# Kernel tuning notes

Measured on AMD Instinct MI355X. Metric: run time of the kernel, lower is better.

## Reference

```python
import jax, jax.numpy as jnp
import numpy as np

B, S, D = 32, 2048, 512
NUM_SEG = 65  # mask//100 in [0, 64]; segment 0 is padding, dropped from output


def setup_inputs() -> dict:
    key = jax.random.key(0)
    k1, k2 = jax.random.split(key)
    output = jax.random.normal(k1, (B, S, D), dtype=jnp.float32)
    mask = jax.random.randint(k2, (B, S), 0, 6500, dtype=jnp.int64)
    return {"output": output, "mask": mask}


def reference(output, mask):
    # torch_scatter.scatter_mean(src=output, index=mask//100, dim=-2)[:, 1:, :]
    seg = mask // 100  # [B, S] segment ids in [0, NUM_SEG)
    sums = jax.vmap(
        lambda o, s: jax.ops.segment_sum(o, s, num_segments=NUM_SEG)
    )(output, seg)  # [B, NUM_SEG, D]
    counts = jax.vmap(
        lambda s: jax.ops.segment_sum(
            jnp.ones(s.shape, dtype=output.dtype), s, num_segments=NUM_SEG
        )
    )(seg)  # [B, NUM_SEG]
    # scatter_mean yields 0 for empty segments; clamping count to 1 preserves that
    mean = sums / jnp.maximum(counts, 1.0)[..., None]
    return mean[:, 1:, :]  # drop segment 0 (padding), -> [B, NUM_SEG-1, D]
```

## Files before the change

kernel.cpp:

```cpp
#include <hip/hip_runtime.h>


constexpr int S = 2048;
constexpr int D = 512;
constexpr int NSEG_OUT = 64;

__global__ __launch_bounds__(256, 8) void seg_mean_kernel(
    const float* __restrict__ src,
    const int* __restrict__ mask,
    float* __restrict__ dst) {
  const int segm1 = blockIdx.x;
  const int b = blockIdx.y;
  const int tid = threadIdx.x;
  const unsigned char myseg = (unsigned char)(segm1 + 1);

  __shared__ unsigned char seg_lds[S];
  __shared__ short list[S];
  __shared__ int mcount;
  __shared__ float combine[D];

  const int4* m4 = (const int4*)(mask + (size_t)b * S);
  #pragma unroll
  for (int it = 0; it < (S / 4) / 256; ++it) {
    const int i = it * 256 + tid;
    const int4 v = m4[i];
    seg_lds[i * 4 + 0] = (unsigned char)(v.x / 100);
    seg_lds[i * 4 + 1] = (unsigned char)(v.y / 100);
    seg_lds[i * 4 + 2] = (unsigned char)(v.z / 100);
    seg_lds[i * 4 + 3] = (unsigned char)(v.w / 100);
  }
  __syncthreads();

  if (tid < 64) {
    int cnt = 0;
    for (int base = 0; base < S; base += 64) {
      const bool match = (seg_lds[base + tid] == myseg);
      const unsigned long long bal = __ballot(match);
      if (match) {
        const int pos = __popcll(bal & ((1ull << tid) - 1ull));
        list[cnt + pos] = (short)(base + tid);
      }
      cnt += __popcll(bal);
    }
    if (tid == 0) mcount = cnt;
  }
  __syncthreads();

  const int m = mcount;
  const int h = tid >> 7;
  const int dt = tid & 127;

  const float4* row4 = (const float4*)(src + (size_t)b * S * D);
  float4 acc = make_float4(0.f, 0.f, 0.f, 0.f);

  int i = h;
  for (; i + 2 < m; i += 4) {
    const int s0 = list[i];
    const int s1 = list[i + 2];
    const float4 v0 = row4[(size_t)s0 * (D / 4) + dt];
    const float4 v1 = row4[(size_t)s1 * (D / 4) + dt];
    acc.x += v0.x; acc.y += v0.y; acc.z += v0.z; acc.w += v0.w;
    acc.x += v1.x; acc.y += v1.y; acc.z += v1.z; acc.w += v1.w;
  }
  if (i < m) {
    const int s0 = list[i];
    const float4 v0 = row4[(size_t)s0 * (D / 4) + dt];
    acc.x += v0.x; acc.y += v0.y; acc.z += v0.z; acc.w += v0.w;
  }

  if (h == 1) {
    ((float4*)combine)[dt] = acc;
  }
  __syncthreads();
  if (h == 0) {
    const float4 o = ((float4*)combine)[dt];
    const float inv = 1.0f / fmaxf((float)m, 1.0f);
    float4 r;
    r.x = (acc.x + o.x) * inv;
    r.y = (acc.y + o.y) * inv;
    r.z = (acc.z + o.z) * inv;
    r.w = (acc.w + o.w) * inv;
    float4* out4 = (float4*)(dst + ((size_t)b * NSEG_OUT + segm1) * D);
    out4[dt] = r;
  }
}

extern "C" void kernel_launch(void* const* d_in, const int* in_sizes, int n_in,
                              void* d_out, int out_size, void* d_ws, size_t ws_size,
                              hipStream_t stream) {
  const float* src = (const float*)d_in[0];
  const int* mask = (const int*)d_in[1];
  float* dst = (float*)d_out;

  dim3 grid(NSEG_OUT, 32);
  seg_mean_kernel<<<grid, 256, 0, stream>>>(src, mask, dst);
}
```

Baseline: 28.98 us.

## Split segment scan and row gather per wavefront to drop block barriers

Each of the four wavefronts now scans its own quarter of the mask with register ballots and builds a private row list, then sums those rows across the full D width. The shared-memory segment-id staging and two block-wide barriers before the gather are removed, leaving one barrier before a final four-way reduction in LDS. The cost is a serial per-match loop in each wave to build the list, plus unbalanced work when matches cluster in one quarter.

```diff
diff --git a/kernel.cpp b/kernel.cpp
--- a/kernel.cpp
+++ b/kernel.cpp
@@ -3,6 +3,7 @@
 
 constexpr int S = 2048;
 constexpr int D = 512;
+constexpr int D4 = D / 4;
 constexpr int NSEG_OUT = 64;
 
 __global__ __launch_bounds__(256, 8) void seg_mean_kernel(
@@ -12,76 +13,88 @@
   const int segm1 = blockIdx.x;
   const int b = blockIdx.y;
   const int tid = threadIdx.x;
-  const unsigned char myseg = (unsigned char)(segm1 + 1);
+  const int w = tid >> 6;
+  const int lane = tid & 63;
+  const int myseg = segm1 + 1;
 
-  __shared__ unsigned char seg_lds[S];
-  __shared__ short list[S];
-  __shared__ int mcount;
-  __shared__ float combine[D];
+  __shared__ float sums[4][D];
+  __shared__ short list[4][512];
+  __shared__ int wcnt[4];
 
-  const int4* m4 = (const int4*)(mask + (size_t)b * S);
+  const int4* m4 = (const int4*)(mask + (size_t)b * S) + (size_t)w * 128;
+  const int4 q0 = m4[lane];
+  const int4 q1 = m4[64 + lane];
+
+  unsigned long long bal[8];
+  bal[0] = __ballot(q0.x / 100 == myseg);
+  bal[1] = __ballot(q0.y / 100 == myseg);
+  bal[2] = __ballot(q0.z / 100 == myseg);
+  bal[3] = __ballot(q0.w / 100 == myseg);
+  bal[4] = __ballot(q1.x / 100 == myseg);
+  bal[5] = __ballot(q1.y / 100 == myseg);
+  bal[6] = __ballot(q1.z / 100 == myseg);
+  bal[7] = __ballot(q1.w / 100 == myseg);
+
+  int cnt = 0;
   #pragma unroll
-  for (int it = 0; it < (S / 4) / 256; ++it) {
-    const int i = it * 256 + tid;
-    const int4 v = m4[i];
-    seg_lds[i * 4 + 0] = (unsigned char)(v.x / 100);
-    seg_lds[i * 4 + 1] = (unsigned char)(v.y / 100);
-    seg_lds[i * 4 + 2] = (unsigned char)(v.z / 100);
-    seg_lds[i * 4 + 3] = (unsigned char)(v.w / 100);
+  for (int r = 0; r < 8; ++r) {
+    unsigned long long bb = bal[r];
+    const int sb = 512 * w + 256 * (r >> 2) + (r & 3);
+    while (bb) {
+      const int L = __ffsll((long long)bb) - 1;
+      bb &= bb - 1;
+      if (lane == 0) list[w][cnt] = (short)(sb + 4 * L);
+      ++cnt;
+    }
   }
+  if (lane == 0) wcnt[w] = cnt;
+
+  const float4* row4 = (const float4*)(src + (size_t)b * S * D);
+  float4 a0 = make_float4(0.f, 0.f, 0.f, 0.f);
+  float4 a1 = make_float4(0.f, 0.f, 0.f, 0.f);
+
+  int i = 0;
+  for (; i + 1 < cnt; i += 2) {
+    const int s0 = list[w][i];
+    const int s1 = list[w][i + 1];
+    const float4* r0 = row4 + (size_t)s0 * D4;
+    const float4* r1 = row4 + (size_t)s1 * D4;
+    const float4 v00 = r0[lane];
+    const float4 v01 = r0[64 + lane];
+    const float4 v10 = r1[lane];
+    const float4 v11 = r1[64 + lane];
+    a0.x += v00.x; a0.y += v00.y; a0.z += v00.z; a0.w += v00.w;
+    a1.x += v01.x; a1.y += v01.y; a1.z += v01.z; a1.w += v01.w;
+    a0.x += v10.x; a0.y += v10.y; a0.z += v10.z; a0.w += v10.w;
+    a1.x += v11.x; a1.y += v11.y; a1.z += v11.z; a1.w += v11.w;
+  }
+  if (i < cnt) {
+    const int s0 = list[w][i];
+    const float4* r0 = row4 + (size_t)s0 * D4;
+    const float4 v00 = r0[lane];
+    const float4 v01 = r0[64 + lane];
+    a0.x += v00.x; a0.y += v00.y; a0.z += v00.z; a0.w += v00.w;
+    a1.x += v01.x; a1.y += v01.y; a1.z += v01.z; a1.w += v01.w;
+  }
+
+  ((float4*)sums[w])[lane] = a0;
+  ((float4*)sums[w])[64 + lane] = a1;
   __syncthreads();
 
-  if (tid < 64) {
-    int cnt = 0;
-    for (int base = 0; base < S; base += 64) {
-      const bool match = (seg_lds[base + tid] == myseg);
-      const unsigned long long bal = __ballot(match);
-      if (match) {
-        const int pos = __popcll(bal & ((1ull << tid) - 1ull));
-        list[cnt + pos] = (short)(base + tid);
-      }
-      cnt += __popcll(bal);
-    }
-    if (tid == 0) mcount = cnt;
-  }
-  __syncthreads();
-
-  const int m = mcount;
-  const int h = tid >> 7;
-  const int dt = tid & 127;
-
-  const float4* row4 = (const float4*)(src + (size_t)b * S * D);
-  float4 acc = make_float4(0.f, 0.f, 0.f, 0.f);
-
-  int i = h;
-  for (; i + 2 < m; i += 4) {
-    const int s0 = list[i];
-    const int s1 = list[i + 2];
-    const float4 v0 = row4[(size_t)s0 * (D / 4) + dt];
-    const float4 v1 = row4[(size_t)s1 * (D / 4) + dt];
-    acc.x += v0.x; acc.y += v0.y; acc.z += v0.z; acc.w += v0.w;
-    acc.x += v1.x; acc.y += v1.y; acc.z += v1.z; acc.w += v1.w;
-  }
-  if (i < m) {
-    const int s0 = list[i];
-    const float4 v0 = row4[(size_t)s0 * (D / 4) + dt];
-    acc.x += v0.x; acc.y += v0.y; acc.z += v0.z; acc.w += v0.w;
-  }
-
-  if (h == 1) {
-    ((float4*)combine)[dt] = acc;
-  }
-  __syncthreads();
-  if (h == 0) {
-    const float4 o = ((float4*)combine)[dt];
+  if (tid < D4) {
+    const int m = wcnt[0] + wcnt[1] + wcnt[2] + wcnt[3];
     const float inv = 1.0f / fmaxf((float)m, 1.0f);
+    const float4 s0 = ((const float4*)sums[0])[tid];
+    const float4 s1 = ((const float4*)sums[1])[tid];
+    const float4 s2 = ((const float4*)sums[2])[tid];
+    const float4 s3 = ((const float4*)sums[3])[tid];
     float4 r;
-    r.x = (acc.x + o.x) * inv;
-    r.y = (acc.y + o.y) * inv;
-    r.z = (acc.z + o.z) * inv;
-    r.w = (acc.w + o.w) * inv;
+    r.x = (s0.x + s1.x + s2.x + s3.x) * inv;
+    r.y = (s0.y + s1.y + s2.y + s3.y) * inv;
+    r.z = (s0.z + s1.z + s2.z + s3.z) * inv;
+    r.w = (s0.w + s1.w + s2.w + s3.w) * inv;
     float4* out4 = (float4*)(dst + ((size_t)b * NSEG_OUT + segm1) * D);
-    out4[dt] = r;
+    out4[tid] = r;
   }
 }
 
```

After: 27.61 us. 4.7% less time.
